# Kernel optimization log

Hardware: AMD Instinct MI355X
Metric: run time of the kernel (lower is better)

The kernel has to match this reference:

```python
import jax, jax.numpy as jnp
import numpy as np

# LightweightConv1d config (matches init_kwargs)
C = 1024        # input_size / channels
H = 16          # num_heads
K = 7           # kernel_size (odd)
PAD = 3         # padding (same-length output)


def setup_inputs() -> dict:
    key = jax.random.key(0)
    kx, kw = jax.random.split(key)
    x = jax.random.normal(kx, (8, 4096, C), dtype=jnp.float32)   # B x T x C
    weight = jax.random.uniform(kw, (H, 1, K), dtype=jnp.float32)  # per-head kernel
    return {"x": x, "weight": weight}


def reference(x, weight):
    # x: (B, T, C); weight: (H, 1, K)
    B, T, _ = x.shape
    # weight softmax over the kernel dimension (weight_softmax=True)
    w = jax.nn.softmax(weight.reshape(H, K), axis=-1)  # (H, K)
    # weight_dropout is identity at inference (eval mode)
    # channel c uses head c % H -> tile head kernels C//H times along channel axis
    w_chan = jnp.tile(w, (C // H, 1))[:, None, :]      # (C, 1, K) depthwise kernel
    x_nct = jnp.transpose(x, (0, 2, 1))                # (B, C, T)
    y = jax.lax.conv_general_dilated(
        x_nct, w_chan,
        window_strides=(1,),
        padding=[(PAD, PAD)],
        dimension_numbers=("NCH", "OIH", "NCH"),
        feature_group_count=C,
    )                                                  # (B, C, T), same length
    return jnp.transpose(y, (0, 2, 1))                 # (B, T, C)
```

## Files before the change

kernel.cpp:

```cpp
#include <hip/hip_runtime.h>


constexpr int B_   = 8;
constexpr int T_   = 4096;
constexpr int C_   = 1024;
constexpr int H_   = 16;
constexpr int K_   = 7;
constexpr int PAD_ = 3;
constexpr int TCHUNK = 8;
constexpr int W_  = TCHUNK + K_ - 1;
constexpr int C4 = C_ / 4;

__global__ __launch_bounds__(256, 4) void lwconv_kernel(
    const float* __restrict__ x, const float* __restrict__ w,
    float* __restrict__ y) {
  __shared__ float ws[H_][K_];
  const int tid = threadIdx.x;

  if (tid < H_) {
    float v[K_];
    float m = -1e30f;
#pragma unroll
    for (int k = 0; k < K_; ++k) { v[k] = w[tid * K_ + k]; m = fmaxf(m, v[k]); }
    float s = 0.f;
#pragma unroll
    for (int k = 0; k < K_; ++k) { v[k] = expf(v[k] - m); s += v[k]; }
    const float inv = 1.f / s;
#pragma unroll
    for (int k = 0; k < K_; ++k) ws[tid][k] = v[k] * inv;
  }
  __syncthreads();

  const int h0 = (4 * tid) & (H_ - 1);
  float wr[4][K_];
#pragma unroll
  for (int j = 0; j < 4; ++j)
#pragma unroll
    for (int k = 0; k < K_; ++k) wr[j][k] = ws[h0 + j][k];

  const int nchunks = T_ / TCHUNK;
  const int b  = blockIdx.x / nchunks;
  const int t0 = (blockIdx.x % nchunks) * TCHUNK;

  const float4* __restrict__ xr =
      reinterpret_cast<const float4*>(x + (size_t)b * T_ * C_) + tid;
  float4* __restrict__ yr =
      reinterpret_cast<float4*>(y + (size_t)b * T_ * C_) + tid;

  const float4 z4 = make_float4(0.f, 0.f, 0.f, 0.f);

  float4 win[W_];
#pragma unroll
  for (int i = 0; i < W_; ++i) {
    const int t = t0 - PAD_ + i;
    win[i] = (t >= 0 && t < T_) ? xr[(size_t)t * C4] : z4;
  }

#pragma unroll
  for (int tt = 0; tt < TCHUNK; ++tt) {
    float ax = 0.f, ay = 0.f, az = 0.f, aw = 0.f;
#pragma unroll
    for (int k = 0; k < K_; ++k) {
      ax = fmaf(win[tt + k].x, wr[0][k], ax);
      ay = fmaf(win[tt + k].y, wr[1][k], ay);
      az = fmaf(win[tt + k].z, wr[2][k], az);
      aw = fmaf(win[tt + k].w, wr[3][k], aw);
    }
    yr[(size_t)(t0 + tt) * C4] = make_float4(ax, ay, az, aw);
  }
}

extern "C" void kernel_launch(void* const* d_in, const int* in_sizes, int n_in,
                              void* d_out, int out_size, void* d_ws, size_t ws_size,
                              hipStream_t stream) {
  const float* x = (const float*)d_in[0];
  const float* w = (const float*)d_in[1];
  float* y = (float*)d_out;

  const int grid = B_ * (T_ / TCHUNK);
  lwconv_kernel<<<grid, 256, 0, stream>>>(x, w, y);
}
```

Baseline: 233.2 us.

## Process 64-step time stripes per block with register-prefetched sliding window

Each block now walks a 64-step time stripe in 8-step chunks, loading the next chunk's rows into registers while computing the current one and sliding the window. This cuts redundant halo reads and per-block softmax setup, and overlaps loads with compute. Output uses nontemporal stores to avoid cache pollution. Risk: the grid shrinks eightfold, lowering parallelism and occupancy.

```diff
diff --git a/kernel.cpp b/kernel.cpp
--- a/kernel.cpp
+++ b/kernel.cpp
@@ -1,17 +1,21 @@
 #include <hip/hip_runtime.h>
 
 
-constexpr int B_   = 8;
-constexpr int T_   = 4096;
-constexpr int C_   = 1024;
-constexpr int H_   = 16;
-constexpr int K_   = 7;
-constexpr int PAD_ = 3;
-constexpr int TCHUNK = 8;
-constexpr int W_  = TCHUNK + K_ - 1;
-constexpr int C4 = C_ / 4;
+typedef float v4f __attribute__((ext_vector_type(4)));
 
-__global__ __launch_bounds__(256, 4) void lwconv_kernel(
+constexpr int B_     = 8;
+constexpr int T_     = 4096;
+constexpr int C_     = 1024;
+constexpr int H_     = 16;
+constexpr int K_     = 7;
+constexpr int PAD_   = 3;
+constexpr int STRIPE = 64;
+constexpr int TCH    = 8;
+constexpr int WIN    = TCH + K_ - 1;
+constexpr int NCHUNK = STRIPE / TCH;
+constexpr int C4     = C_ / 4;
+
+__global__ __launch_bounds__(256) void lwconv_kernel(
     const float* __restrict__ x, const float* __restrict__ w,
     float* __restrict__ y) {
   __shared__ float ws[H_][K_];
@@ -38,36 +42,57 @@
 #pragma unroll
     for (int k = 0; k < K_; ++k) wr[j][k] = ws[h0 + j][k];
 
-  const int nchunks = T_ / TCHUNK;
-  const int b  = blockIdx.x / nchunks;
-  const int t0 = (blockIdx.x % nchunks) * TCHUNK;
+  const int stripes = T_ / STRIPE;
+  const int b  = blockIdx.x / stripes;
+  const int s0 = (blockIdx.x % stripes) * STRIPE;
 
-  const float4* __restrict__ xr =
-      reinterpret_cast<const float4*>(x + (size_t)b * T_ * C_) + tid;
-  float4* __restrict__ yr =
-      reinterpret_cast<float4*>(y + (size_t)b * T_ * C_) + tid;
+  const v4f* __restrict__ xr =
+      reinterpret_cast<const v4f*>(x + (size_t)b * T_ * C_) + tid;
+  v4f* __restrict__ yr =
+      reinterpret_cast<v4f*>(y + (size_t)b * T_ * C_) + tid;
 
-  const float4 z4 = make_float4(0.f, 0.f, 0.f, 0.f);
+  const v4f z4 = {0.f, 0.f, 0.f, 0.f};
 
-  float4 win[W_];
+  v4f win[WIN];
 #pragma unroll
-  for (int i = 0; i < W_; ++i) {
-    const int t = t0 - PAD_ + i;
+  for (int i = 0; i < WIN; ++i) {
+    const int t = s0 - PAD_ + i;
     win[i] = (t >= 0 && t < T_) ? xr[(size_t)t * C4] : z4;
   }
 
+  v4f nxt[TCH];
+
+  auto compute_chunk = [&](int t0) {
 #pragma unroll
-  for (int tt = 0; tt < TCHUNK; ++tt) {
-    float ax = 0.f, ay = 0.f, az = 0.f, aw = 0.f;
+    for (int tt = 0; tt < TCH; ++tt) {
+      float ax = 0.f, ay = 0.f, az = 0.f, aw = 0.f;
 #pragma unroll
-    for (int k = 0; k < K_; ++k) {
-      ax = fmaf(win[tt + k].x, wr[0][k], ax);
-      ay = fmaf(win[tt + k].y, wr[1][k], ay);
-      az = fmaf(win[tt + k].z, wr[2][k], az);
-      aw = fmaf(win[tt + k].w, wr[3][k], aw);
+      for (int k = 0; k < K_; ++k) {
+        ax = fmaf(win[tt + k].x, wr[0][k], ax);
+        ay = fmaf(win[tt + k].y, wr[1][k], ay);
+        az = fmaf(win[tt + k].z, wr[2][k], az);
+        aw = fmaf(win[tt + k].w, wr[3][k], aw);
+      }
+      const v4f out = {ax, ay, az, aw};
+      __builtin_nontemporal_store(out, &yr[(size_t)(t0 + tt) * C4]);
     }
-    yr[(size_t)(t0 + tt) * C4] = make_float4(ax, ay, az, aw);
+  };
+
+#pragma unroll 1
+  for (int chunk = 0; chunk < NCHUNK - 1; ++chunk) {
+    const int t0 = s0 + chunk * TCH;
+#pragma unroll
+    for (int i = 0; i < TCH; ++i) {
+      const int t = t0 + (WIN - PAD_) + i;
+      nxt[i] = (t < T_) ? xr[(size_t)t * C4] : z4;
+    }
+    compute_chunk(t0);
+#pragma unroll
+    for (int i = 0; i < WIN - TCH; ++i) win[i] = win[i + TCH];
+#pragma unroll
+    for (int i = 0; i < TCH; ++i) win[WIN - TCH + i] = nxt[i];
   }
+  compute_chunk(s0 + (NCHUNK - 1) * TCH);
 }
 
 extern "C" void kernel_launch(void* const* d_in, const int* in_sizes, int n_in,
@@ -77,6 +102,6 @@
   const float* w = (const float*)d_in[1];
   float* y = (float*)d_out;
 
-  const int grid = B_ * (T_ / TCHUNK);
+  const int grid = B_ * (T_ / STRIPE);
   lwconv_kernel<<<grid, 256, 0, stream>>>(x, w, y);
 }
```

New measurement: 236.0 us. About the same (+1.2%).
